# Kernel tuning notes

Measured on AMD Instinct MI355X. Metric: run time of the kernel, lower is better.

Reference implementation:

```python
import jax, jax.numpy as jnp
import numpy as np

B, S, D = 8, 2048, 512

def setup_inputs() -> dict:
    key = jax.random.key(0)
    k1, k2 = jax.random.split(key)
    lstm_out = jax.random.normal(k1, (B, S, D), dtype=jnp.float32)
    # xavier_uniform init for [D, D]
    limit = float(np.sqrt(6.0 / (D + D)))
    attention_weights = jax.random.uniform(k2, (D, D), dtype=jnp.float32, minval=-limit, maxval=limit)
    return {"lstm_out": lstm_out, "attention_weights": attention_weights}

def reference(lstm_out, attention_weights):
    # scores[b,i,j] = tanh( (x W) x^T )
    proj = jnp.einsum('bsd,de->bse', lstm_out, attention_weights)          # [B,S,D]
    scores = jnp.tanh(jnp.einsum('bsd,btd->bst', proj, lstm_out))          # [B,S,S]
    attn = jax.nn.softmax(scores, axis=-1)                                 # [B,S,S]
    return jnp.einsum('bst,btd->bsd', attn, lstm_out)                      # [B,S,D]
```

## Files before the change

### kernel.cpp

```cpp
#include <hip/hip_runtime.h>
#include <hip/hip_bf16.h>

typedef __bf16 bf16;
typedef __attribute__((ext_vector_type(8))) __bf16 bf16x8;
typedef __attribute__((ext_vector_type(4))) __bf16 bf16x4;
typedef __attribute__((ext_vector_type(4))) float floatx4;

__device__ __forceinline__ void gl_lds16(const bf16* g, bf16* l) {
    __builtin_amdgcn_global_load_lds(
        (const __attribute__((address_space(1))) unsigned int*)g,
        (__attribute__((address_space(3))) unsigned int*)l,
        16, 0, 0);
}

__global__ __launch_bounds__(256) void cast_f32_bf16_v4(const float* __restrict__ in,
                                                        bf16* __restrict__ out,
                                                        long long n4) {
    long long i = (long long)blockIdx.x * 256 + threadIdx.x;
    if (i < n4) {
        float4 v = ((const float4*)in)[i];
        bf16x4 o;
        o[0] = (bf16)v.x; o[1] = (bf16)v.y; o[2] = (bf16)v.z; o[3] = (bf16)v.w;
        ((bf16x4*)out)[i] = o;
    }
}

__global__ __launch_bounds__(256) void cast_transpose(const float* __restrict__ in,
                                                      bf16* __restrict__ out,
                                                      int R, int C) {
    __shared__ float tile[32][33];
    const long long bz = blockIdx.z;
    in  += bz * (long long)R * C;
    out += bz * (long long)R * C;
    const int r0 = blockIdx.x * 32, c0 = blockIdx.y * 32;
    const int tx = threadIdx.x & 31, ty = threadIdx.x >> 5;
#pragma unroll
    for (int i = 0; i < 32; i += 8)
        tile[ty + i][tx] = in[(long long)(r0 + ty + i) * C + (c0 + tx)];
    __syncthreads();
#pragma unroll
    for (int i = 0; i < 32; i += 8)
        out[(long long)(c0 + ty + i) * R + (r0 + tx)] = (bf16)tile[tx][ty + i];
}

__device__ __forceinline__ float fast_tanh(float v) {
    float e = __expf(2.0f * v);
    return 1.0f - 2.0f / (e + 1.0f);
}

template <int MODE>
__global__ __launch_bounds__(256) void gemm128_nt(const bf16* __restrict__ A,
                                                  const bf16* __restrict__ Bm,
                                                  void* __restrict__ Cout,
                                                  float* __restrict__ rowsum,
                                                  int M, int N, int K,
                                                  long long batchA, long long batchB,
                                                  long long batchC, long long batchR) {
    const long long bz = blockIdx.z;
    A  += bz * batchA;
    Bm += bz * batchB;

    __shared__ __align__(16) char lds_raw[34816];
    bf16* As = (bf16*)lds_raw;
    bf16* Bs = As + 128 * 32;

    const int t    = threadIdx.x;
    const int lane = t & 63;
    const int wave = t >> 6;
    const int quad = lane >> 4;
    const int l16  = lane & 15;

    const int m0 = blockIdx.x * 128;
    const int n0 = blockIdx.y * 128;
    const int wm = (wave >> 1) * 64;
    const int wn = (wave & 1) * 64;

    floatx4 acc[4][4] = {};

    const int r0 = t >> 2;
    const int c0 = (t & 3) * 8;

    const bf16* Ag0 = A + (long long)(m0 + r0) * K + c0;
    const bf16* Ag1 = A + (long long)(m0 + 64 + r0) * K + c0;
    const bf16* Bg0 = Bm + (long long)(n0 + r0) * K + c0;
    const bf16* Bg1 = Bm + (long long)(n0 + 64 + r0) * K + c0;

    for (int k0 = 0; k0 < K; k0 += 32) {
        gl_lds16(Ag0 + k0, &As[t * 8]);
        gl_lds16(Ag1 + k0, &As[(t + 256) * 8]);
        gl_lds16(Bg0 + k0, &Bs[t * 8]);
        gl_lds16(Bg1 + k0, &Bs[(t + 256) * 8]);
        __syncthreads();

        bf16x8 af[4], bfr[4];
#pragma unroll
        for (int i = 0; i < 4; ++i)
            af[i] = *(const bf16x8*)(&As[(wm + i * 16 + l16) * 32 + quad * 8]);
#pragma unroll
        for (int j = 0; j < 4; ++j)
            bfr[j] = *(const bf16x8*)(&Bs[(wn + j * 16 + l16) * 32 + quad * 8]);

#pragma unroll
        for (int i = 0; i < 4; ++i)
#pragma unroll
            for (int j = 0; j < 4; ++j)
                acc[i][j] = __builtin_amdgcn_mfma_f32_16x16x32_bf16(af[i], bfr[j], acc[i][j], 0, 0, 0);

        __syncthreads();
    }

    if (MODE == 0 || MODE == 1) {
        bf16* Cb = (bf16*)lds_raw;
        float ps[4][4];
#pragma unroll
        for (int i = 0; i < 4; ++i)
#pragma unroll
            for (int r = 0; r < 4; ++r) ps[i][r] = 0.f;

#pragma unroll
        for (int i = 0; i < 4; ++i)
#pragma unroll
            for (int j = 0; j < 4; ++j)
#pragma unroll
                for (int r = 0; r < 4; ++r) {
                    float v = acc[i][j][r];
                    if (MODE == 1) { v = __expf(fast_tanh(v)); ps[i][r] += v; }
                    Cb[(wm + i * 16 + quad * 4 + r) * 136 + (wn + j * 16 + l16)] = (bf16)v;
                }

        if (MODE == 1) {
#pragma unroll
            for (int i = 0; i < 4; ++i)
#pragma unroll
                for (int r = 0; r < 4; ++r) {
                    float s = ps[i][r];
#pragma unroll
                    for (int msk = 1; msk < 16; msk <<= 1) s += __shfl_xor(s, msk);
                    if (l16 == 0)
                        atomicAdd(&rowsum[bz * batchR + m0 + wm + i * 16 + quad * 4 + r], s);
                }
        }
        __syncthreads();
        bf16* Cg = (bf16*)Cout + bz * batchC;
#pragma unroll
        for (int c = 0; c < 8; ++c) {
            int ch  = t + c * 256;
            int row = ch >> 4, k16 = ch & 15;
            bf16x8 pk = *(const bf16x8*)&Cb[row * 136 + k16 * 8];
            *(bf16x8*)(Cg + (long long)(m0 + row) * N + n0 + k16 * 8) = pk;
        }
    } else {
        float* Cf = (float*)lds_raw;
        float* rs = (float*)lds_raw + 64 * 132;
        if (t < 128) rs[t] = rowsum[bz * batchR + m0 + t];
        __syncthreads();
        float* Og = (float*)Cout + bz * batchC;
#pragma unroll
        for (int half = 0; half < 2; ++half) {
            if (wm == half * 64) {
#pragma unroll
                for (int i = 0; i < 4; ++i)
#pragma unroll
                    for (int r = 0; r < 4; ++r) {
                        int rl = i * 16 + quad * 4 + r;
                        float inv = 1.0f / rs[half * 64 + rl];
#pragma unroll
                        for (int j = 0; j < 4; ++j)
                            Cf[rl * 132 + (wn + j * 16 + l16)] = acc[i][j][r] * inv;
                    }
            }
            __syncthreads();
#pragma unroll
            for (int c = 0; c < 8; ++c) {
                int ch  = t + c * 256;
                int row = ch >> 5, c4 = ch & 31;
                floatx4 pk = *(const floatx4*)&Cf[row * 132 + c4 * 4];
                *(floatx4*)(Og + (long long)(m0 + half * 64 + row) * N + n0 + c4 * 4) = pk;
            }
            __syncthreads();
        }
    }
}

extern "C" void kernel_launch(void* const* d_in, const int* in_sizes, int n_in,
                              void* d_out, int out_size, void* d_ws, size_t ws_size,
                              hipStream_t stream) {
    const int B = 8, S = 2048, D = 512;
    const float* x = (const float*)d_in[0];
    const float* W = (const float*)d_in[1];
    float* out = (float*)d_out;

    const size_t nx = (size_t)B * S * D;
    const size_t nw = (size_t)D * D;

    char* ws = (char*)d_ws;
    auto al = [](size_t v) { return (v + 255) & ~(size_t)255; };
    size_t off = 0;
    bf16* xb = (bf16*)(ws + off); off = al(off + nx * 2);
    bf16* xt = (bf16*)(ws + off); off = al(off + nx * 2);
    bf16* pb = (bf16*)(ws + off); off = al(off + nx * 2);
    bf16* wt = (bf16*)(ws + off); off = al(off + nw * 2);
    float* rsum = (float*)(ws + off); off = al(off + (size_t)B * S * 4);
    bf16* sb = (bf16*)(ws + off);
    const size_t full_need = off + (size_t)B * S * S * 2;
    const bool batched = (ws_size >= full_need);

    hipMemsetAsync(rsum, 0, (size_t)B * S * 4, stream);

    cast_f32_bf16_v4<<<(int)((nx / 4 + 255) / 256), 256, 0, stream>>>(x, xb, (long long)(nx / 4));
    { dim3 g(S / 32, D / 32, B); cast_transpose<<<g, 256, 0, stream>>>(x, xt, S, D); }
    { dim3 g(D / 32, D / 32, 1); cast_transpose<<<g, 256, 0, stream>>>(W, wt, D, D); }

    {
        dim3 g(B * S / 128, D / 128, 1);
        gemm128_nt<0><<<g, 256, 0, stream>>>(xb, wt, (void*)pb, nullptr, B * S, D, D, 0, 0, 0, 0);
    }

    const long long sd = (long long)S * D;
    const long long ss = (long long)S * S;

    if (batched) {
        dim3 g2(S / 128, S / 128, B);
        gemm128_nt<1><<<g2, 256, 0, stream>>>(pb, xb, (void*)sb, rsum, S, S, D, sd, sd, ss, S);
        dim3 g4(S / 128, D / 128, B);
        gemm128_nt<2><<<g4, 256, 0, stream>>>(sb, xt, (void*)out, rsum, S, D, S, ss, sd, sd, S);
    } else {
        for (int b = 0; b < B; ++b) {
            dim3 g2(S / 128, S / 128, 1);
            gemm128_nt<1><<<g2, 256, 0, stream>>>(pb + (size_t)b * sd, xb + (size_t)b * sd,
                                                  (void*)sb, rsum + (size_t)b * S, S, S, D, 0, 0, 0, 0);
            dim3 g4(S / 128, D / 128, 1);
            gemm128_nt<2><<<g4, 256, 0, stream>>>(sb, xt + (size_t)b * sd,
                                                  (void*)(out + (size_t)b * sd), rsum + (size_t)b * S,
                                                  S, D, S, 0, 0, 0, 0);
        }
    }
}
```

Before: 248.8 us.

## Fuse x cast with transpose and drop LDS-staged GEMM epilogue

Combines the plain bf16 cast and the transposed bf16 cast of x into one kernel that reads x once. In the GEMM kernels, the epilogue now writes accumulator values directly to global memory instead of staging them through LDS for vectorized stores, which removes barriers and cuts LDS use. The trade-off is narrow, less coalesced 2- or 4-byte stores, especially on the large score matrix.

Measured after the change: 233.7 us. -6.0%, faster.

```diff
diff --git a/kernel.cpp b/kernel.cpp
--- a/kernel.cpp
+++ b/kernel.cpp
@@ -13,25 +13,33 @@
         16, 0, 0);
 }
 
-__global__ __launch_bounds__(256) void cast_f32_bf16_v4(const float* __restrict__ in,
-                                                        bf16* __restrict__ out,
-                                                        long long n4) {
-    long long i = (long long)blockIdx.x * 256 + threadIdx.x;
-    if (i < n4) {
-        float4 v = ((const float4*)in)[i];
-        bf16x4 o;
-        o[0] = (bf16)v.x; o[1] = (bf16)v.y; o[2] = (bf16)v.z; o[3] = (bf16)v.w;
-        ((bf16x4*)out)[i] = o;
-    }
+__global__ __launch_bounds__(256) void cast_both(const float* __restrict__ in,
+                                                 bf16* __restrict__ outn,
+                                                 bf16* __restrict__ outt,
+                                                 int R, int C) {
+    __shared__ float tile[32][33];
+    const long long bz = blockIdx.z;
+    in   += bz * (long long)R * C;
+    outn += bz * (long long)R * C;
+    outt += bz * (long long)R * C;
+    const int r0 = blockIdx.x * 32, c0 = blockIdx.y * 32;
+    const int tx = threadIdx.x & 31, ty = threadIdx.x >> 5;
+#pragma unroll
+    for (int i = 0; i < 32; i += 8) {
+        float v = in[(long long)(r0 + ty + i) * C + (c0 + tx)];
+        tile[ty + i][tx] = v;
+        outn[(long long)(r0 + ty + i) * C + (c0 + tx)] = (bf16)v;
+    }
+    __syncthreads();
+#pragma unroll
+    for (int i = 0; i < 32; i += 8)
+        outt[(long long)(c0 + ty + i) * R + (r0 + tx)] = (bf16)tile[tx][ty + i];
 }
 
 __global__ __launch_bounds__(256) void cast_transpose(const float* __restrict__ in,
                                                       bf16* __restrict__ out,
                                                       int R, int C) {
     __shared__ float tile[32][33];
-    const long long bz = blockIdx.z;
-    in  += bz * (long long)R * C;
-    out += bz * (long long)R * C;
     const int r0 = blockIdx.x * 32, c0 = blockIdx.y * 32;
     const int tx = threadIdx.x & 31, ty = threadIdx.x >> 5;
 #pragma unroll
@@ -60,9 +68,9 @@
     A  += bz * batchA;
     Bm += bz * batchB;
 
-    __shared__ __align__(16) char lds_raw[34816];
-    bf16* As = (bf16*)lds_raw;
-    bf16* Bs = As + 128 * 32;
+    __shared__ bf16 As[128 * 32];
+    __shared__ bf16 Bs[128 * 32];
+    __shared__ float rs[128];
 
     const int t    = threadIdx.x;
     const int lane = t & 63;
@@ -110,7 +118,7 @@
     }
 
     if (MODE == 0 || MODE == 1) {
-        bf16* Cb = (bf16*)lds_raw;
+        bf16* Cg = (bf16*)Cout + bz * batchC;
         float ps[4][4];
 #pragma unroll
         for (int i = 0; i < 4; ++i)
@@ -125,7 +133,9 @@
                 for (int r = 0; r < 4; ++r) {
                     float v = acc[i][j][r];
                     if (MODE == 1) { v = __expf(fast_tanh(v)); ps[i][r] += v; }
-                    Cb[(wm + i * 16 + quad * 4 + r) * 136 + (wn + j * 16 + l16)] = (bf16)v;
+                    long long row = m0 + wm + i * 16 + quad * 4 + r;
+                    long long col = n0 + wn + j * 16 + l16;
+                    Cg[row * (long long)N + col] = (bf16)v;
                 }
 
         if (MODE == 1) {
@@ -140,45 +150,22 @@
                         atomicAdd(&rowsum[bz * batchR + m0 + wm + i * 16 + quad * 4 + r], s);
                 }
         }
-        __syncthreads();
-        bf16* Cg = (bf16*)Cout + bz * batchC;
-#pragma unroll
-        for (int c = 0; c < 8; ++c) {
-            int ch  = t + c * 256;
-            int row = ch >> 4, k16 = ch & 15;
-            bf16x8 pk = *(const bf16x8*)&Cb[row * 136 + k16 * 8];
-            *(bf16x8*)(Cg + (long long)(m0 + row) * N + n0 + k16 * 8) = pk;
-        }
     } else {
-        float* Cf = (float*)lds_raw;
-        float* rs = (float*)lds_raw + 64 * 132;
         if (t < 128) rs[t] = rowsum[bz * batchR + m0 + t];
         __syncthreads();
         float* Og = (float*)Cout + bz * batchC;
 #pragma unroll
-        for (int half = 0; half < 2; ++half) {
-            if (wm == half * 64) {
-#pragma unroll
-                for (int i = 0; i < 4; ++i)
-#pragma unroll
-                    for (int r = 0; r < 4; ++r) {
-                        int rl = i * 16 + quad * 4 + r;
-                        float inv = 1.0f / rs[half * 64 + rl];
-#pragma unroll
-                        for (int j = 0; j < 4; ++j)
-                            Cf[rl * 132 + (wn + j * 16 + l16)] = acc[i][j][r] * inv;
-                    }
+        for (int i = 0; i < 4; ++i)
+#pragma unroll
+            for (int r = 0; r < 4; ++r) {
+                float inv = 1.0f / rs[wm + i * 16 + quad * 4 + r];
+                long long row = m0 + wm + i * 16 + quad * 4 + r;
+#pragma unroll
+                for (int j = 0; j < 4; ++j) {
+                    long long col = n0 + wn + j * 16 + l16;
+                    Og[row * (long long)N + col] = acc[i][j][r] * inv;
+                }
             }
-            __syncthreads();
-#pragma unroll
-            for (int c = 0; c < 8; ++c) {
-                int ch  = t + c * 256;
-                int row = ch >> 5, c4 = ch & 31;
-                floatx4 pk = *(const floatx4*)&Cf[row * 132 + c4 * 4];
-                *(floatx4*)(Og + (long long)(m0 + half * 64 + row) * N + n0 + c4 * 4) = pk;
-            }
-            __syncthreads();
-        }
     }
 }
 
@@ -207,8 +194,7 @@
 
     hipMemsetAsync(rsum, 0, (size_t)B * S * 4, stream);
 
-    cast_f32_bf16_v4<<<(int)((nx / 4 + 255) / 256), 256, 0, stream>>>(x, xb, (long long)(nx / 4));
-    { dim3 g(S / 32, D / 32, B); cast_transpose<<<g, 256, 0, stream>>>(x, xt, S, D); }
+    { dim3 g(S / 32, D / 32, B); cast_both<<<g, 256, 0, stream>>>(x, xb, xt, S, D); }
     { dim3 g(D / 32, D / 32, 1); cast_transpose<<<g, 256, 0, stream>>>(W, wt, D, D); }
 
     {
```
